# Kernel tuning notes

Measured on AMD Instinct MI355X. Metric: run time of the kernel, lower is better.

## Reference

```python
import jax
import jax.numpy as jnp
import numpy as np
from jax import lax


def setup_inputs() -> dict:
    key = jax.random.key(0)
    k0, k1 = jax.random.split(key)
    B, C, H, W = 8, 256, 96, 96
    FM0 = jax.random.normal(k0, (B, C, H, W), dtype=jnp.float32)
    FM1 = jax.random.normal(k1, (B, C, H, W), dtype=jnp.float32)
    return {"FM0": FM0, "FM1": FM1, "d_max": 4, "stride": 1}


def pointwise_correlation(FM0, FM1, d_max, stride):
    """out[b,h,w,i,j] = sum_c FM0[b,c,h,w] * FM1[b,c,h+(i-d)*s, w+(j-d)*s],
    with zero padding outside FM1's spatial extent."""
    B, C, H, W = FM0.shape
    D = 2 * d_max + 1
    p = d_max * stride
    FM1p = jnp.pad(FM1, ((0, 0), (0, 0), (p, p), (p, p)))
    offs = jnp.arange(D, dtype=jnp.int32) * stride  # start offsets into padded map
    ys, xs = jnp.meshgrid(offs, offs, indexing="ij")
    offsets = jnp.stack([ys.ravel(), xs.ravel()], axis=-1)  # (D*D, 2)

    def step(carry, off):
        sl = lax.dynamic_slice(FM1p, (0, 0, off[0], off[1]), (B, C, H, W))
        corr = jnp.einsum("bchw,bchw->bhw", FM0, sl)
        return carry, corr

    _, out = lax.scan(step, None, offsets)  # (D*D, B, H, W)
    out = out.reshape(D, D, B, H, W).transpose(2, 3, 4, 0, 1)  # (B, H, W, D, D)
    return out


def reference(FM0, FM1, d_max, stride):
    return pointwise_correlation(FM0, FM1, d_max, stride)
```

## Files before the change

### kernel.cpp

```cpp
#include <hip/hip_runtime.h>

#define HH 96
#define WW 96
#define CC 256
#define PLANE (HH * WW)
#define PITCH 40
#define AROWS 144
#define BROWS 704
#define NGRP 1696
#define NOUT 81

typedef __attribute__((ext_vector_type(4))) float f32x4;
typedef __attribute__((ext_vector_type(2))) unsigned int u32x2;
typedef __attribute__((ext_vector_type(8))) __bf16 bf16x8;

static __device__ __forceinline__ unsigned int pkbf(float x, float y) {
  unsigned int ux = __builtin_bit_cast(unsigned int, x) + 0x8000u;
  unsigned int uy = __builtin_bit_cast(unsigned int, y) + 0x8000u;
  return __builtin_amdgcn_perm(uy, ux, 0x07060302u);
}

__global__ __launch_bounds__(384, 2) void corr_kernel(
    const float* __restrict__ fm0, const float* __restrict__ fm1,
    float* __restrict__ out) {
  __shared__ __align__(16) unsigned short lds[(AROWS + BROWS) * PITCH];

  const int tid = threadIdx.x;
  const int bid = blockIdx.x;
  const int b = bid & 7;
  const int q = bid >> 3;
  const int s = q & 1;
  const int h0 = 3 * (q >> 1);

  const int lane = tid & 63;
  const int wv = tid >> 6;
  const int mm = lane & 15;
  const int kg = lane >> 4;

  const size_t boff = (size_t)b * CC * PLANE;

  if (wv >= 3) {
    const int pt = tid - 192;
    const float* gptr[9];
    int gdst[9];
    bool gact[9], gok[9];
    #pragma unroll
    for (int j = 0; j < 9; ++j) {
      const int g = pt + 192 * j;
      gact[j] = (g < NGRP);
      if (g < 288) {
        const int a = g / 96, r = g % 96;
        const int wq = r >> 3, cq = r & 7;
        const int wst = 48 * s + 4 * wq;
        gok[j] = gact[j];
        gdst[j] = (a * 48 + 4 * wq) * PITCH + 4 * cq;
        gptr[j] = fm0 + boff + (size_t)(4 * cq) * PLANE + (h0 + a) * WW + wst;
      } else {
        const int gb = g - 288;
        const int i = gb >> 7, r = gb & 127;
        const int wq = r >> 3, cq = r & 7;
        const int hb = h0 - 4 + i;
        const int wst = 48 * s - 8 + 4 * wq;
        const bool ok = (hb >= 0) && (hb < HH) && (wst >= 0) && (wst < WW);
        gok[j] = ok && gact[j];
        gdst[j] = (AROWS + i * 64 + 4 * wq) * PITCH + 4 * cq;
        gptr[j] = fm1 + boff + (size_t)(4 * cq) * PLANE +
                  (size_t)(ok ? hb : 0) * WW + (ok ? wst : 0);
      }
    }
    f32x4 pre[9][4];
    #pragma unroll
    for (int j = 0; j < 9; ++j)
      #pragma unroll
      for (int cc = 0; cc < 4; ++cc) pre[j][cc] = f32x4{0.f, 0.f, 0.f, 0.f};
    #pragma unroll
    for (int j = 0; j < 9; ++j)
      if (gok[j]) {
        #pragma unroll
        for (int cc = 0; cc < 4; ++cc)
          pre[j][cc] = *(const f32x4*)(gptr[j] + (size_t)cc * PLANE);
      }

    #pragma unroll 1
    for (int ks = 0; ks < 8; ++ks) {
      __syncthreads();
      #pragma unroll
      for (int j = 0; j < 9; ++j)
        if (gact[j]) {
          #pragma unroll
          for (int dw = 0; dw < 4; ++dw) {
            u32x2 v;
            v.x = pkbf(pre[j][0][dw], pre[j][1][dw]);
            v.y = pkbf(pre[j][2][dw], pre[j][3][dw]);
            *(u32x2*)&lds[gdst[j] + dw * PITCH] = v;
          }
        }
      if (ks < 7) {
        const size_t koff = (size_t)((ks + 1) * 32) * PLANE;
        #pragma unroll
        for (int j = 0; j < 9; ++j)
          if (gok[j]) {
            #pragma unroll
            for (int cc = 0; cc < 4; ++cc)
              pre[j][cc] = *(const f32x4*)(gptr[j] + koff + (size_t)cc * PLANE);
          }
      }
      __syncthreads();
    }
  } else {
    f32x4 acc[9][3][2];
    #pragma unroll
    for (int i = 0; i < 9; ++i)
      #pragma unroll
      for (int mt = 0; mt < 3; ++mt) {
        acc[i][mt][0] = f32x4{0.f, 0.f, 0.f, 0.f};
        acc[i][mt][1] = f32x4{0.f, 0.f, 0.f, 0.f};
      }
    const int abase = (wv * 48 + mm) * PITCH + kg * 8;
    const int bbase = (AROWS + mm) * PITCH + kg * 8;

    #pragma unroll 1
    for (int ks = 0; ks < 8; ++ks) {
      __syncthreads();
      __syncthreads();
      bf16x8 af[3];
      #pragma unroll
      for (int mt = 0; mt < 3; ++mt)
        af[mt] = *(const bf16x8*)&lds[abase + 16 * mt * PITCH];
      #pragma unroll
      for (int i = 0; i < 9; ++i) {
        const int bb = bbase + (wv + i) * 64 * PITCH;
        bf16x8 b0 = *(const bf16x8*)&lds[bb];
        #pragma unroll
        for (int mt = 0; mt < 3; ++mt) {
          bf16x8 b1 = *(const bf16x8*)&lds[bb + 16 * (mt + 1) * PITCH];
          acc[i][mt][0] = __builtin_amdgcn_mfma_f32_16x16x32_bf16(af[mt], b0, acc[i][mt][0], 0, 0, 0);
          acc[i][mt][1] = __builtin_amdgcn_mfma_f32_16x16x32_bf16(af[mt], b1, acc[i][mt][1], 0, 0, 0);
          b0 = b1;
        }
      }
    }

    float* outb = out + ((size_t)b * PLANE + (size_t)(h0 + wv) * WW) * NOUT;
    #pragma unroll
    for (int u = 0; u < 2; ++u)
      #pragma unroll
      for (int rg = 0; rg < 4; ++rg) {
        const int j = 16 * u + mm - 4 * kg - rg - 4;
        if ((unsigned)j < 9u) {
          #pragma unroll
          for (int i = 0; i < 9; ++i)
            #pragma unroll
            for (int mt = 0; mt < 3; ++mt) {
              const int w = 48 * s + 16 * mt + 4 * kg + rg;
              outb[(size_t)w * NOUT + i * 9 + j] = acc[i][mt][u][rg];
            }
        }
      }
  }
}

extern "C" void kernel_launch(void* const* d_in, const int* in_sizes, int n_in,
                              void* d_out, int out_size, void* d_ws, size_t ws_size,
                              hipStream_t stream) {
  const float* fm0 = (const float*)d_in[0];
  const float* fm1 = (const float*)d_in[1];
  float* out = (float*)d_out;
  corr_kernel<<<dim3(512), dim3(384), 0, stream>>>(fm0, fm1, out);
}
```

Measured before the change: 215.8 us.

## Retile correlation to 4x32 tiles with double-buffered LDS and finer channel pipeline

```diff
diff --git a/kernel.cpp b/kernel.cpp
--- a/kernel.cpp
+++ b/kernel.cpp
@@ -5,9 +5,9 @@
 #define CC 256
 #define PLANE (HH * WW)
 #define PITCH 40
-#define AROWS 144
-#define BROWS 704
-#define NGRP 1696
+#define ROWS 704
+#define BUFW (ROWS * PITCH)
+#define NGRP 704
 #define NOUT 81
 
 typedef __attribute__((ext_vector_type(4))) float f32x4;
@@ -20,128 +20,170 @@
   return __builtin_amdgcn_perm(uy, ux, 0x07060302u);
 }
 
-__global__ __launch_bounds__(384, 2) void corr_kernel(
+#define BAR_LGKM() do { __builtin_amdgcn_s_waitcnt(0xC07F); __builtin_amdgcn_s_barrier(); } while (0)
+
+__global__ __launch_bounds__(512, 2) void corr_kernel(
     const float* __restrict__ fm0, const float* __restrict__ fm1,
     float* __restrict__ out) {
-  __shared__ __align__(16) unsigned short lds[(AROWS + BROWS) * PITCH];
+  __shared__ __align__(16) unsigned short lds[2 * BUFW];
 
   const int tid = threadIdx.x;
   const int bid = blockIdx.x;
   const int b = bid & 7;
-  const int q = bid >> 3;
-  const int s = q & 1;
-  const int h0 = 3 * (q >> 1);
+  const int r = bid >> 3;
+  const int s = r % 3;
+  const int h0 = 4 * (r / 3);
 
   const int lane = tid & 63;
-  const int wv = tid >> 6;
   const int mm = lane & 15;
   const int kg = lane >> 4;
-
   const size_t boff = (size_t)b * CC * PLANE;
 
-  if (wv >= 3) {
-    const int pt = tid - 192;
-    const float* gptr[9];
-    int gdst[9];
-    bool gact[9], gok[9];
-    #pragma unroll
-    for (int j = 0; j < 9; ++j) {
-      const int g = pt + 192 * j;
+  if (tid >= 256) {
+    const int pt = tid - 256;
+    int gdst[3];
+    const float* gsrc[3];
+    bool gact[3], gok[3];
+    #pragma unroll
+    for (int j = 0; j < 3; ++j) {
+      const int g = pt + 256 * j;
       gact[j] = (g < NGRP);
-      if (g < 288) {
-        const int a = g / 96, r = g % 96;
-        const int wq = r >> 3, cq = r & 7;
-        const int wst = 48 * s + 4 * wq;
-        gok[j] = gact[j];
-        gdst[j] = (a * 48 + 4 * wq) * PITCH + 4 * cq;
-        gptr[j] = fm0 + boff + (size_t)(4 * cq) * PLANE + (h0 + a) * WW + wst;
+      const int gg = gact[j] ? g : 0;
+      int row, cq, hh, wg;
+      const float* src;
+      bool ok;
+      if (gg < 128) {
+        const int wq = gg & 7, a = (gg >> 3) & 3;
+        cq = gg >> 5;
+        row = a * 32 + 4 * wq;
+        hh = h0 + a;
+        wg = 32 * s + 4 * wq;
+        src = fm0;
+        ok = true;
       } else {
-        const int gb = g - 288;
-        const int i = gb >> 7, r = gb & 127;
-        const int wq = r >> 3, cq = r & 7;
-        const int hb = h0 - 4 + i;
-        const int wst = 48 * s - 8 + 4 * wq;
-        const bool ok = (hb >= 0) && (hb < HH) && (wst >= 0) && (wst < WW);
-        gok[j] = ok && gact[j];
-        gdst[j] = (AROWS + i * 64 + 4 * wq) * PITCH + 4 * cq;
-        gptr[j] = fm1 + boff + (size_t)(4 * cq) * PLANE +
-                  (size_t)(ok ? hb : 0) * WW + (ok ? wst : 0);
-      }
-    }
-    f32x4 pre[9][4];
-    #pragma unroll
-    for (int j = 0; j < 9; ++j)
+        const int gb = gg - 128;
+        const int wq = gb % 12, t2 = gb / 12;
+        const int i = t2 % 12;
+        cq = t2 / 12;
+        row = 128 + i * 48 + 4 * wq;
+        hh = h0 - 4 + i;
+        wg = 32 * s - 8 + 4 * wq;
+        src = fm1;
+        ok = (hh >= 0) && (hh < HH) && (wg >= 0) && (wg <= WW - 4);
+      }
+      gok[j] = ok && gact[j];
+      gdst[j] = row * PITCH + 4 * cq;
+      gsrc[j] = src + boff + (size_t)(4 * cq) * PLANE + (ok ? (hh * WW + wg) : 0);
+    }
+
+    f32x4 pre[3][4];
+    #pragma unroll
+    for (int j = 0; j < 3; ++j)
       #pragma unroll
       for (int cc = 0; cc < 4; ++cc) pre[j][cc] = f32x4{0.f, 0.f, 0.f, 0.f};
     #pragma unroll
-    for (int j = 0; j < 9; ++j)
+    for (int j = 0; j < 3; ++j)
       if (gok[j]) {
         #pragma unroll
         for (int cc = 0; cc < 4; ++cc)
-          pre[j][cc] = *(const f32x4*)(gptr[j] + (size_t)cc * PLANE);
+          pre[j][cc] = *(const f32x4*)(gsrc[j] + (size_t)cc * PLANE);
       }
 
     #pragma unroll 1
-    for (int ks = 0; ks < 8; ++ks) {
-      __syncthreads();
-      #pragma unroll
-      for (int j = 0; j < 9; ++j)
+    for (int hf = 0; hf < 16; ++hf) {
+      BAR_LGKM();
+      const int base = ((hf >> 1) & 1) * BUFW + (hf & 1) * 16;
+      #pragma unroll
+      for (int j = 0; j < 3; ++j)
         if (gact[j]) {
           #pragma unroll
           for (int dw = 0; dw < 4; ++dw) {
             u32x2 v;
             v.x = pkbf(pre[j][0][dw], pre[j][1][dw]);
             v.y = pkbf(pre[j][2][dw], pre[j][3][dw]);
-            *(u32x2*)&lds[gdst[j] + dw * PITCH] = v;
+            *(u32x2*)&lds[base + gdst[j] + dw * PITCH] = v;
           }
         }
-      if (ks < 7) {
-        const size_t koff = (size_t)((ks + 1) * 32) * PLANE;
+      if (hf < 15) {
+        const size_t coff = (size_t)(16 * (hf + 1)) * PLANE;
         #pragma unroll
-        for (int j = 0; j < 9; ++j)
+        for (int j = 0; j < 3; ++j)
           if (gok[j]) {
             #pragma unroll
             for (int cc = 0; cc < 4; ++cc)
-              pre[j][cc] = *(const f32x4*)(gptr[j] + koff + (size_t)cc * PLANE);
-          }
-      }
-      __syncthreads();
-    }
+              pre[j][cc] = *(const f32x4*)(gsrc[j] + coff + (size_t)cc * PLANE);
+          }
+      }
+    }
+    BAR_LGKM();
   } else {
-    f32x4 acc[9][3][2];
+    const int a = tid >> 6;
+    f32x4 acc[9][2][2];
     #pragma unroll
     for (int i = 0; i < 9; ++i)
       #pragma unroll
-      for (int mt = 0; mt < 3; ++mt) {
+      for (int mt = 0; mt < 2; ++mt) {
         acc[i][mt][0] = f32x4{0.f, 0.f, 0.f, 0.f};
         acc[i][mt][1] = f32x4{0.f, 0.f, 0.f, 0.f};
       }
-    const int abase = (wv * 48 + mm) * PITCH + kg * 8;
-    const int bbase = (AROWS + mm) * PITCH + kg * 8;
+    bf16x8 af0, af1;
+    const int arow = (a * 32 + mm) * PITCH + kg * 8;
+    const int brow = (128 + a * 48 + mm) * PITCH + kg * 8;
 
     #pragma unroll 1
-    for (int ks = 0; ks < 8; ++ks) {
-      __syncthreads();
-      __syncthreads();
-      bf16x8 af[3];
-      #pragma unroll
-      for (int mt = 0; mt < 3; ++mt)
-        af[mt] = *(const bf16x8*)&lds[abase + 16 * mt * PITCH];
+    for (int hf = 0; hf < 16; ++hf) {
+      BAR_LGKM();
+      const int c = hf - 2;
+      if (c >= 0) {
+        const int bufb = ((c >> 1) & 1) * BUFW;
+        if (!(c & 1)) {
+          af0 = *(const bf16x8*)&lds[bufb + arow];
+          af1 = *(const bf16x8*)&lds[bufb + arow + 16 * PITCH];
+          #pragma unroll
+          for (int i = 0; i < 4; ++i) {
+            const int bb = bufb + brow + i * 48 * PITCH;
+            bf16x8 b0 = *(const bf16x8*)&lds[bb];
+            bf16x8 b1 = *(const bf16x8*)&lds[bb + 16 * PITCH];
+            bf16x8 b2 = *(const bf16x8*)&lds[bb + 32 * PITCH];
+            acc[i][0][0] = __builtin_amdgcn_mfma_f32_16x16x32_bf16(af0, b0, acc[i][0][0], 0, 0, 0);
+            acc[i][0][1] = __builtin_amdgcn_mfma_f32_16x16x32_bf16(af0, b1, acc[i][0][1], 0, 0, 0);
+            acc[i][1][0] = __builtin_amdgcn_mfma_f32_16x16x32_bf16(af1, b1, acc[i][1][0], 0, 0, 0);
+            acc[i][1][1] = __builtin_amdgcn_mfma_f32_16x16x32_bf16(af1, b2, acc[i][1][1], 0, 0, 0);
+          }
+        } else {
+          #pragma unroll
+          for (int i = 4; i < 9; ++i) {
+            const int bb = bufb + brow + i * 48 * PITCH;
+            bf16x8 b0 = *(const bf16x8*)&lds[bb];
+            bf16x8 b1 = *(const bf16x8*)&lds[bb + 16 * PITCH];
+            bf16x8 b2 = *(const bf16x8*)&lds[bb + 32 * PITCH];
+            acc[i][0][0] = __builtin_amdgcn_mfma_f32_16x16x32_bf16(af0, b0, acc[i][0][0], 0, 0, 0);
+            acc[i][0][1] = __builtin_amdgcn_mfma_f32_16x16x32_bf16(af0, b1, acc[i][0][1], 0, 0, 0);
+            acc[i][1][0] = __builtin_amdgcn_mfma_f32_16x16x32_bf16(af1, b1, acc[i][1][0], 0, 0, 0);
+            acc[i][1][1] = __builtin_amdgcn_mfma_f32_16x16x32_bf16(af1, b2, acc[i][1][1], 0, 0, 0);
+          }
+        }
+      }
+    }
+    BAR_LGKM();
+    {
+      const int bufb = BUFW;
+      af0 = *(const bf16x8*)&lds[bufb + arow];
+      af1 = *(const bf16x8*)&lds[bufb + arow + 16 * PITCH];
       #pragma unroll
       for (int i = 0; i < 9; ++i) {
-        const int bb = bbase + (wv + i) * 64 * PITCH;
+        const int bb = bufb + brow + i * 48 * PITCH;
         bf16x8 b0 = *(const bf16x8*)&lds[bb];
-        #pragma unroll
-        for (int mt = 0; mt < 3; ++mt) {
-          bf16x8 b1 = *(const bf16x8*)&lds[bb + 16 * (mt + 1) * PITCH];
-          acc[i][mt][0] = __builtin_amdgcn_mfma_f32_16x16x32_bf16(af[mt], b0, acc[i][mt][0], 0, 0, 0);
-          acc[i][mt][1] = __builtin_amdgcn_mfma_f32_16x16x32_bf16(af[mt], b1, acc[i][mt][1], 0, 0, 0);
-          b0 = b1;
-        }
-      }
-    }
-
-    float* outb = out + ((size_t)b * PLANE + (size_t)(h0 + wv) * WW) * NOUT;
+        bf16x8 b1 = *(const bf16x8*)&lds[bb + 16 * PITCH];
+        bf16x8 b2 = *(const bf16x8*)&lds[bb + 32 * PITCH];
+        acc[i][0][0] = __builtin_amdgcn_mfma_f32_16x16x32_bf16(af0, b0, acc[i][0][0], 0, 0, 0);
+        acc[i][0][1] = __builtin_amdgcn_mfma_f32_16x16x32_bf16(af0, b1, acc[i][0][1], 0, 0, 0);
+        acc[i][1][0] = __builtin_amdgcn_mfma_f32_16x16x32_bf16(af1, b1, acc[i][1][0], 0, 0, 0);
+        acc[i][1][1] = __builtin_amdgcn_mfma_f32_16x16x32_bf16(af1, b2, acc[i][1][1], 0, 0, 0);
+      }
+    }
+
+    float* outb = out + ((size_t)b * PLANE + (size_t)(h0 + a) * WW) * NOUT;
     #pragma unroll
     for (int u = 0; u < 2; ++u)
       #pragma unroll
@@ -149,12 +191,12 @@
         const int j = 16 * u + mm - 4 * kg - rg - 4;
         if ((unsigned)j < 9u) {
           #pragma unroll
-          for (int i = 0; i < 9; ++i)
+          for (int mt = 0; mt < 2; ++mt) {
+            const int w = 32 * s + 16 * mt + 4 * kg + rg;
             #pragma unroll
-            for (int mt = 0; mt < 3; ++mt) {
-              const int w = 48 * s + 16 * mt + 4 * kg + rg;
+            for (int i = 0; i < 9; ++i)
               outb[(size_t)w * NOUT + i * 9 + j] = acc[i][mt][u][rg];
-            }
+          }
         }
       }
   }
@@ -166,5 +208,5 @@
   const float* fm0 = (const float*)d_in[0];
   const float* fm1 = (const float*)d_in[1];
   float* out = (float*)d_out;
-  corr_kernel<<<dim3(512), dim3(384), 0, stream>>>(fm0, fm1, out);
+  corr_kernel<<<dim3(576), dim3(512), 0, stream>>>(fm0, fm1, out);
 }
```

After: 243.6 us. 12.9% more time.
